# Optimization experiments

Hardware: AMD Instinct MI355X
Metric: run time of the kernel (lower is better)

The kernel has to match this reference:

```python
import jax, jax.numpy as jnp
import numpy as np

DIM = 1024
SEQ = 4096


def setup_inputs() -> dict:
    key = jax.random.key(0)
    ks = jax.random.split(key, 7)
    s = 1.0 / np.sqrt(DIM)
    return {
        "X": jax.random.normal(ks[0], (SEQ, DIM), dtype=jnp.float32),
        "Wq": jax.random.uniform(ks[1], (DIM, DIM), jnp.float32, -s, s),
        "bq": jax.random.uniform(ks[2], (DIM,), jnp.float32, -s, s),
        "Wk": jax.random.uniform(ks[3], (DIM, DIM), jnp.float32, -s, s),
        "bk": jax.random.uniform(ks[4], (DIM,), jnp.float32, -s, s),
        "Wv": jax.random.uniform(ks[5], (DIM, DIM), jnp.float32, -s, s),
        "bv": jax.random.uniform(ks[6], (DIM,), jnp.float32, -s, s),
    }


def reference(X, Wq, bq, Wk, bk, Wv, bv):
    # QKV projections (nn.Linear: x @ W.T + b); here W stored as [in, out]
    Q = X @ Wq + bq            # [S, D]
    K = X @ Wk + bk            # [S, D]
    V = X @ Wv + bv            # [S, D]
    scale = 1.0 / jnp.sqrt(jnp.asarray(X.shape[-1], X.dtype))
    scores = (Q @ K.T) * scale  # [S, S]
    attn = jax.nn.softmax(scores, axis=-1)
    return attn @ V            # [S, D]
```

## Files before the change

### kernel.cpp

```cpp
#include <hip/hip_runtime.h>

typedef unsigned short u16;
typedef unsigned int u32;
typedef __bf16 bf16x8 __attribute__((ext_vector_type(8)));
typedef float f32x4 __attribute__((ext_vector_type(4)));
typedef u16 u16x4 __attribute__((ext_vector_type(4)));

__device__ __forceinline__ u16 f32_to_bf16(float f) {
    u32 u = __builtin_bit_cast(u32, f);
    u32 r = (u + 0x7fffu + ((u >> 16) & 1u)) >> 16;
    return (u16)r;
}

__device__ __forceinline__ float bf16_to_f32(u16 h) {
    u32 u = (u32)h << 16;
    return __builtin_bit_cast(float, u);
}

__device__ __forceinline__ void async_cp16(const u16* g, u16* l) {
    __builtin_amdgcn_global_load_lds(
        (const __attribute__((address_space(1))) u32*)g,
        (__attribute__((address_space(3))) u32*)l, 16, 0, 0);
}

#define G2_DECL(Aptr, Bptr, LDA, LDB, KLEN)                                   \
    __shared__ u16 lds[65536];                                                \
    const int tid  = threadIdx.x;                                             \
    const int wid  = tid >> 6;                                                \
    const int lane = tid & 63;                                                \
    const int wr = wid >> 2;                 \
    const int wc = wid & 3;                  \
    const int row16 = lane & 15;                                              \
    const int quad  = lane >> 4;                                              \
    const int sc0 = (quad * 8) ^ ((row16 & 7) * 8);       \
    const int gr = lane >> 3;                           \
    const int gc = ((lane & 7) ^ gr) * 8;               \
    const int blk0 = wid * 2, blk1 = blk0 + 1;                                \
    const size_t ldaS = (LDA), ldbS = (LDB);                                  \
    const u16* gA = (Aptr) + (size_t)(bm + gr) * ldaS + gc;                   \
    const u16* gB = (Bptr) + (size_t)(bn + gr) * ldbS + gc;                   \
    const int NT = (KLEN) >> 6;                                               \
    f32x4 acc[8][4];                                                          \
    {                                                                         \
        const f32x4 z_ = {0.f, 0.f, 0.f, 0.f};                                \
        _Pragma("unroll")                                                     \
        for (int i_ = 0; i_ < 8; i_++)                                        \
            _Pragma("unroll")                                                 \
            for (int j_ = 0; j_ < 4; j_++) acc[i_][j_] = z_;                  \
    }

#define G2_STAGE(bsel) {                                                      \
    u16* l_ = &lds[(bsel) * 32768];                                           \
    async_cp16(gA + (size_t)(blk0 * 8) * ldaS,       l_ + blk0 * 512);        \
    async_cp16(gA + (size_t)(blk1 * 8) * ldaS,       l_ + blk1 * 512);        \
    async_cp16(gA + (size_t)(128 + blk0 * 8) * ldaS, l_ + 8192 + blk0 * 512); \
    async_cp16(gA + (size_t)(128 + blk1 * 8) * ldaS, l_ + 8192 + blk1 * 512); \
    async_cp16(gB + (size_t)(blk0 * 8) * ldbS,       l_ + 16384 + blk0 * 512);\
    async_cp16(gB + (size_t)(blk1 * 8) * ldbS,       l_ + 16384 + blk1 * 512);\
    async_cp16(gB + (size_t)(128 + blk0 * 8) * ldbS, l_ + 24576 + blk0 * 512);\
    async_cp16(gB + (size_t)(128 + blk1 * 8) * ldbS, l_ + 24576 + blk1 * 512);\
    gA += 64; gB += 64; }

#define G2_LA(cb, im, sc) \
    (*(const bf16x8*)&lds[(cb) + wr * 8192 + (im) * 1024 + row16 * 64 + (sc)])
#define G2_LB(cb, in, sc) \
    (*(const bf16x8*)&lds[(cb) + 16384 + wc * 4096 + (in) * 1024 + row16 * 64 + (sc)])

#define G2_MMA(IM0, JN0, FB)                                                  \
    _Pragma("unroll")                                                         \
    for (int i_m = 0; i_m < 4; i_m++)                                         \
        _Pragma("unroll")                                                     \
        for (int j_n = 0; j_n < 2; j_n++) {                                   \
            acc[(IM0) + i_m][(JN0) + j_n] =                                   \
                __builtin_amdgcn_mfma_f32_16x16x32_bf16(                      \
                    fa[i_m][0], FB[j_n][0], acc[(IM0) + i_m][(JN0) + j_n],    \
                    0, 0, 0);                                                 \
            acc[(IM0) + i_m][(JN0) + j_n] =                                   \
                __builtin_amdgcn_mfma_f32_16x16x32_bf16(                      \
                    fa[i_m][1], FB[j_n][1], acc[(IM0) + i_m][(JN0) + j_n],    \
                    0, 0, 0);                                                 \
        }

#define G2_KLOOP()                                                            \
    G2_STAGE(0)                                                               \
    G2_STAGE(1)                                                               \
    for (int t = 0; t < NT; t++) {                                            \
        const int cb = (t & 1) * 32768;                                       \
        if (t < NT - 1) { asm volatile("s_waitcnt vmcnt(8)" ::: "memory"); }  \
        else            { asm volatile("s_waitcnt vmcnt(0)" ::: "memory"); }  \
        __builtin_amdgcn_s_barrier();                                         \
        bf16x8 fa[4][2], f0[2][2], f1[2][2];                                  \
                                 \
        _Pragma("unroll")                                                     \
        for (int i = 0; i < 4; i++) {                                         \
            fa[i][0] = G2_LA(cb, i, sc0);                                     \
            fa[i][1] = G2_LA(cb, i, sc0 ^ 32);                                \
        }                                                                     \
        _Pragma("unroll")                                                     \
        for (int j = 0; j < 2; j++) {                                         \
            f0[j][0] = G2_LB(cb, j, sc0);                                     \
            f0[j][1] = G2_LB(cb, j, sc0 ^ 32);                                \
        }                                                                     \
        __builtin_amdgcn_s_barrier();                                         \
        __builtin_amdgcn_s_setprio(1);                                        \
        G2_MMA(0, 0, f0)                                                      \
        __builtin_amdgcn_s_setprio(0);                                        \
        __builtin_amdgcn_s_barrier();                                         \
                                           \
        _Pragma("unroll")                                                     \
        for (int j = 0; j < 2; j++) {                                         \
            f1[j][0] = G2_LB(cb, 2 + j, sc0);                                 \
            f1[j][1] = G2_LB(cb, 2 + j, sc0 ^ 32);                            \
        }                                                                     \
        __builtin_amdgcn_s_barrier();                                         \
        __builtin_amdgcn_s_setprio(1);                                        \
        G2_MMA(0, 2, f1)                                                      \
        __builtin_amdgcn_s_setprio(0);                                        \
        __builtin_amdgcn_s_barrier();                                         \
                               \
        _Pragma("unroll")                                                     \
        for (int i = 0; i < 4; i++) {                                         \
            fa[i][0] = G2_LA(cb, 4 + i, sc0);                                 \
            fa[i][1] = G2_LA(cb, 4 + i, sc0 ^ 32);                            \
        }                                                                     \
        __builtin_amdgcn_s_barrier();                                         \
        __builtin_amdgcn_s_setprio(1);                                        \
        G2_MMA(4, 2, f1)                                                      \
        __builtin_amdgcn_s_setprio(0);                                        \
        __builtin_amdgcn_s_barrier();                                         \
                                    \
        _Pragma("unroll")                                                     \
        for (int j = 0; j < 2; j++) {                                         \
            f0[j][0] = G2_LB(cb, j, sc0);                                     \
            f0[j][1] = G2_LB(cb, j, sc0 ^ 32);                                \
        }                                                                     \
        __builtin_amdgcn_s_barrier();                                         \
        __builtin_amdgcn_s_setprio(1);                                        \
        G2_MMA(4, 0, f0)                                                      \
        __builtin_amdgcn_s_setprio(0);                                        \
        asm volatile("s_waitcnt lgkmcnt(0)" ::: "memory");                    \
        __builtin_amdgcn_s_barrier();                                         \
        if (t + 2 < NT) { G2_STAGE((t & 1)) }                                 \
    }

__global__ __launch_bounds__(512, 2)
void gemm_qkv(const u16* __restrict__ A, const u16* __restrict__ B,
              u16* __restrict__ C, u16* __restrict__ Vt,
              const float* __restrict__ bias,
              int K, int lda, int ldb, int ldc)
{
    const int L  = blockIdx.x;
    const int wg = (L & 7) * 24 + (L >> 3);
    const int bm = (wg / 12) * 256;
    const int bn = (wg % 12) * 256;
    G2_DECL(A, B, lda, ldb, K)
    G2_KLOOP()
    if (bn < 2048) {
        #pragma unroll
        for (int im = 0; im < 8; im++) {
            #pragma unroll
            for (int in = 0; in < 4; in++) {
                const int n = bn + wc * 64 + in * 16 + row16;
                const float bv = bias[n];
                #pragma unroll
                for (int r = 0; r < 4; r++) {
                    const int m = bm + wr * 128 + im * 16 + quad * 4 + r;
                    C[(size_t)m * ldc + n] = f32_to_bf16(acc[im][in][r] + bv);
                }
            }
        }
    } else {
        #pragma unroll
        for (int im = 0; im < 8; im++) {
            #pragma unroll
            for (int in = 0; in < 4; in++) {
                const int n = bn + wc * 64 + in * 16 + row16;
                const float bv = bias[n];
                const int d = n - 2048;
                const int m = bm + wr * 128 + im * 16 + quad * 4;
                u16x4 pk;
                #pragma unroll
                for (int r = 0; r < 4; r++)
                    pk[r] = f32_to_bf16(acc[im][in][r] + bv);
                *(u16x4*)&Vt[(size_t)d * 4096 + m] = pk;
            }
        }
    }
}

__global__ __launch_bounds__(512, 2)
void gemm_score_exp(const u16* __restrict__ A, const u16* __restrict__ B,
                    u16* __restrict__ P, float* __restrict__ rowsum,
                    int K, int lda, int ldb, int ldc, float scale)
{
    const int L = blockIdx.x;
    const int xcd = L & 7, q = L >> 3;
    const int bm = ((xcd >> 1) * 4 + (q >> 3)) * 256;
    const int bn = ((xcd & 1) * 8 + (q & 7)) * 256;
    G2_DECL(A, B, lda, ldb, K)
    G2_KLOOP()
    #pragma unroll
    for (int im = 0; im < 8; im++) {
        #pragma unroll
        for (int r = 0; r < 4; r++) {
            const int m = bm + wr * 128 + im * 16 + quad * 4 + r;
            float rs = 0.f;
            #pragma unroll
            for (int in = 0; in < 4; in++) {
                const int n = bn + wc * 64 + in * 16 + row16;
                float e = __expf(acc[im][in][r] * scale);
                P[(size_t)m * ldc + n] = f32_to_bf16(e);
                rs += e;
            }
            rs += __shfl_xor(rs, 1);
            rs += __shfl_xor(rs, 2);
            rs += __shfl_xor(rs, 4);
            rs += __shfl_xor(rs, 8);
            if (row16 == 0) atomicAdd(&rowsum[m], rs);
        }
    }
}

__global__ __launch_bounds__(512, 2)
void gemm_pv_splitk(const u16* __restrict__ A, const u16* __restrict__ B,
                    u16* __restrict__ P0, u16* __restrict__ P1,
                    u16* __restrict__ P2, u16* __restrict__ P3,
                    int Kq, int lda, int ldb, int ldc)
{
    const int L = blockIdx.x;
    const int xcd = L & 7, q = L >> 3;
    const int bm = ((xcd >> 1) * 4 + (q & 3)) * 256;
    const int bn = ((xcd & 1) * 2 + (q >> 2)) * 256;
    const int z  = blockIdx.y;
    u16* C = (z == 0) ? P0 : (z == 1) ? P1 : (z == 2) ? P2 : P3;
    const int koff = z * Kq;
    G2_DECL(A + koff, B + koff, lda, ldb, Kq)
    G2_KLOOP()
    #pragma unroll
    for (int im = 0; im < 8; im++) {
        #pragma unroll
        for (int in = 0; in < 4; in++) {
            const int n = bn + wc * 64 + in * 16 + row16;
            #pragma unroll
            for (int r = 0; r < 4; r++) {
                const int m = bm + wr * 128 + im * 16 + quad * 4 + r;
                C[(size_t)m * ldc + n] = f32_to_bf16(acc[im][in][r]);
            }
        }
    }
}

__global__ __launch_bounds__(256)
void reduce4_scale(float4* __restrict__ out, const u16x4* __restrict__ p0,
                   const u16x4* __restrict__ p1, const u16x4* __restrict__ p2,
                   const u16x4* __restrict__ p3, const float* __restrict__ rowsum)
{
    const int i = blockIdx.x * 256 + threadIdx.x;
    const float inv = 1.0f / rowsum[i >> 8];
    u16x4 a = p0[i], b = p1[i], c = p2[i], d = p3[i];
    float4 o;
    o.x = (bf16_to_f32(a[0]) + bf16_to_f32(b[0]) + bf16_to_f32(c[0]) + bf16_to_f32(d[0])) * inv;
    o.y = (bf16_to_f32(a[1]) + bf16_to_f32(b[1]) + bf16_to_f32(c[1]) + bf16_to_f32(d[1])) * inv;
    o.z = (bf16_to_f32(a[2]) + bf16_to_f32(b[2]) + bf16_to_f32(c[2]) + bf16_to_f32(d[2])) * inv;
    o.w = (bf16_to_f32(a[3]) + bf16_to_f32(b[3]) + bf16_to_f32(c[3]) + bf16_to_f32(d[3])) * inv;
    out[i] = o;
}

__global__ __launch_bounds__(256)
void prep_all(const float4* __restrict__ X, uint2* __restrict__ Xb,
              const float* __restrict__ W0, const float* __restrict__ W1,
              const float* __restrict__ W2, u16* __restrict__ Wt,
              const float* __restrict__ bq, const float* __restrict__ bk,
              const float* __restrict__ bv, float* __restrict__ b3,
              float* __restrict__ rowsum)
{
    __shared__ float t[32][33];
    const int b = blockIdx.x;
    if (b < 4096) {
        const int i = b * 256 + threadIdx.x;
        float4 v = X[i];
        uint2 o;
        o.x = (u32)f32_to_bf16(v.x) | ((u32)f32_to_bf16(v.y) << 16);
        o.y = (u32)f32_to_bf16(v.z) | ((u32)f32_to_bf16(v.w) << 16);
        Xb[i] = o;
    } else if (b < 7168) {
        const int tt = b - 4096;
        const int z  = tt >> 10;
        const int r  = tt & 1023;
        const float* W = (z == 0) ? W0 : (z == 1) ? W1 : W2;
        u16* dst = Wt + (size_t)z * 1024 * 1024;
        const int bk2 = (r & 31) * 32;
        const int bn2 = (r >> 5) * 32;
        const int tx = threadIdx.x & 31;
        const int ty = threadIdx.x >> 5;
        #pragma unroll
        for (int i = 0; i < 32; i += 8)
            t[ty + i][tx] = W[(size_t)(bk2 + ty + i) * 1024 + bn2 + tx];
        __syncthreads();
        #pragma unroll
        for (int i = 0; i < 32; i += 8)
            dst[(size_t)(bn2 + ty + i) * 1024 + bk2 + tx] = f32_to_bf16(t[tx][ty + i]);
    } else {
        const int i = (b - 7168) * 256 + threadIdx.x;
        if (i < 3072)
            b3[i] = (i < 1024) ? bq[i] : (i < 2048) ? bk[i - 1024] : bv[i - 2048];
        else
            rowsum[i - 3072] = 0.f;
    }
}

extern "C" void kernel_launch(void* const* d_in, const int* in_sizes, int n_in,
                              void* d_out, int out_size, void* d_ws, size_t ws_size,
                              hipStream_t stream)
{
    const float* X  = (const float*)d_in[0];
    const float* Wq = (const float*)d_in[1];
    const float* bq = (const float*)d_in[2];
    const float* Wk = (const float*)d_in[3];
    const float* bk = (const float*)d_in[4];
    const float* Wv = (const float*)d_in[5];
    const float* bv = (const float*)d_in[6];
    float* out = (float*)d_out;

    char* ws = (char*)d_ws;
    u16*   P      = (u16*)ws;
    u16*   Xb     = (u16*)ws;
    u16*   WqkvT  = (u16*)(ws + (8u << 20));
    float* rowsum = (float*)(ws + (32u << 20));
    float* bias3  = (float*)(ws + (32u << 20) + (64u << 10));
    u16*   QKV    = (u16*)(ws + (33u << 20));
    u16*   p0     = (u16*)(ws + (33u << 20));
    u16*   p1     = (u16*)(ws + (41u << 20));
    u16*   p2     = (u16*)(ws + (49u << 20));
    u16*   p3     = (u16*)(ws + (57u << 20));
    u16*   Vt     = (u16*)(ws + (65u << 20));

    prep_all<<<7196, 256, 0, stream>>>((const float4*)X, (uint2*)Xb,
        Wq, Wk, Wv, WqkvT, bq, bk, bv, bias3, rowsum);

    gemm_qkv<<<192, 512, 0, stream>>>(Xb, WqkvT, QKV, Vt, bias3,
        1024, 1024, 1024, 3072);

    gemm_score_exp<<<256, 512, 0, stream>>>(QKV, QKV + 1024, P, rowsum,
        1024, 3072, 3072, 4096, 0.03125f);

    gemm_pv_splitk<<<dim3(64, 4), 512, 0, stream>>>(P, Vt, p0, p1, p2, p3,
        1024, 4096, 4096, 1024);

    reduce4_scale<<<4096, 256, 0, stream>>>((float4*)out, (const u16x4*)p0,
        (const u16x4*)p1, (const u16x4*)p2, (const u16x4*)p3, rowsum);
}
```

Measured before the change: 222.3 us.

## Interleave next-tile async loads across MMA phases and reuse B fragments

Restructures the GEMM K-loop so that the global-to-LDS copies for the next tile are spread across the three MFMA phases of the current tile, instead of being issued in a batch at the end of each iteration with two tiles in flight. The loop is unrolled by two with fixed LDS buffer offsets. The fourth phase now reuses the f0 fragments already held in registers instead of reloading them from LDS, which removes one LDS read pass and one barrier. The trade-off is that prefetch depth drops from two tiles to one, and each tile ends with a full vmcnt(0) wait, which can expose global load latency.

```diff
diff --git a/kernel.cpp b/kernel.cpp
--- a/kernel.cpp
+++ b/kernel.cpp
@@ -49,17 +49,10 @@
             for (int j_ = 0; j_ < 4; j_++) acc[i_][j_] = z_;                  \
     }
 
-#define G2_STAGE(bsel) {                                                      \
-    u16* l_ = &lds[(bsel) * 32768];                                           \
-    async_cp16(gA + (size_t)(blk0 * 8) * ldaS,       l_ + blk0 * 512);        \
-    async_cp16(gA + (size_t)(blk1 * 8) * ldaS,       l_ + blk1 * 512);        \
-    async_cp16(gA + (size_t)(128 + blk0 * 8) * ldaS, l_ + 8192 + blk0 * 512); \
-    async_cp16(gA + (size_t)(128 + blk1 * 8) * ldaS, l_ + 8192 + blk1 * 512); \
-    async_cp16(gB + (size_t)(blk0 * 8) * ldbS,       l_ + 16384 + blk0 * 512);\
-    async_cp16(gB + (size_t)(blk1 * 8) * ldbS,       l_ + 16384 + blk1 * 512);\
-    async_cp16(gB + (size_t)(128 + blk0 * 8) * ldbS, l_ + 24576 + blk0 * 512);\
-    async_cp16(gB + (size_t)(128 + blk1 * 8) * ldbS, l_ + 24576 + blk1 * 512);\
-    gA += 64; gB += 64; }
+#define G2_ST_A(NB, R, LOFF) \
+    async_cp16(gA + (size_t)(R) * ldaS, &lds[(NB) + (LOFF)]);
+#define G2_ST_B(NB, R, LOFF) \
+    async_cp16(gB + (size_t)(R) * ldbS, &lds[(NB) + 16384 + (LOFF)]);
 
 #define G2_LA(cb, im, sc) \
     (*(const bf16x8*)&lds[(cb) + wr * 8192 + (im) * 1024 + row16 * 64 + (sc)])
@@ -81,66 +74,86 @@
                     0, 0, 0);                                                 \
         }
 
-#define G2_KLOOP()                                                            \
-    G2_STAGE(0)                                                               \
-    G2_STAGE(1)                                                               \
-    for (int t = 0; t < NT; t++) {                                            \
-        const int cb = (t & 1) * 32768;                                       \
-        if (t < NT - 1) { asm volatile("s_waitcnt vmcnt(8)" ::: "memory"); }  \
-        else            { asm volatile("s_waitcnt vmcnt(0)" ::: "memory"); }  \
-        __builtin_amdgcn_s_barrier();                                         \
+#define G2_TILE(CB, NB, SCOND)                                                \
+    {                                                                         \
         bf16x8 fa[4][2], f0[2][2], f1[2][2];                                  \
-                                 \
+          \
         _Pragma("unroll")                                                     \
         for (int i = 0; i < 4; i++) {                                         \
-            fa[i][0] = G2_LA(cb, i, sc0);                                     \
-            fa[i][1] = G2_LA(cb, i, sc0 ^ 32);                                \
+            fa[i][0] = G2_LA(CB, i, sc0);                                     \
+            fa[i][1] = G2_LA(CB, i, sc0 ^ 32);                                \
         }                                                                     \
         _Pragma("unroll")                                                     \
         for (int j = 0; j < 2; j++) {                                         \
-            f0[j][0] = G2_LB(cb, j, sc0);                                     \
-            f0[j][1] = G2_LB(cb, j, sc0 ^ 32);                                \
+            f0[j][0] = G2_LB(CB, j, sc0);                                     \
+            f0[j][1] = G2_LB(CB, j, sc0 ^ 32);                                \
+        }                                                                     \
+        if (SCOND) {                                                          \
+            G2_ST_A(NB, blk0 * 8, blk0 * 512)                                 \
+            G2_ST_A(NB, blk1 * 8, blk1 * 512)                                 \
+            G2_ST_A(NB, 128 + blk0 * 8, 8192 + blk0 * 512)                    \
         }                                                                     \
         __builtin_amdgcn_s_barrier();                                         \
         __builtin_amdgcn_s_setprio(1);                                        \
         G2_MMA(0, 0, f0)                                                      \
         __builtin_amdgcn_s_setprio(0);                                        \
         __builtin_amdgcn_s_barrier();                                         \
-                                           \
+                  \
         _Pragma("unroll")                                                     \
         for (int j = 0; j < 2; j++) {                                         \
-            f1[j][0] = G2_LB(cb, 2 + j, sc0);                                 \
-            f1[j][1] = G2_LB(cb, 2 + j, sc0 ^ 32);                            \
+            f1[j][0] = G2_LB(CB, 2 + j, sc0);                                 \
+            f1[j][1] = G2_LB(CB, 2 + j, sc0 ^ 32);                            \
+        }                                                                     \
+        if (SCOND) {                                                          \
+            G2_ST_A(NB, 128 + blk1 * 8, 8192 + blk1 * 512)                    \
+            G2_ST_B(NB, blk0 * 8, blk0 * 512)                                 \
+            G2_ST_B(NB, blk1 * 8, blk1 * 512)                                 \
         }                                                                     \
         __builtin_amdgcn_s_barrier();                                         \
         __builtin_amdgcn_s_setprio(1);                                        \
         G2_MMA(0, 2, f1)                                                      \
         __builtin_amdgcn_s_setprio(0);                                        \
         __builtin_amdgcn_s_barrier();                                         \
-                               \
+                  \
         _Pragma("unroll")                                                     \
         for (int i = 0; i < 4; i++) {                                         \
-            fa[i][0] = G2_LA(cb, 4 + i, sc0);                                 \
-            fa[i][1] = G2_LA(cb, 4 + i, sc0 ^ 32);                            \
+            fa[i][0] = G2_LA(CB, 4 + i, sc0);                                 \
+            fa[i][1] = G2_LA(CB, 4 + i, sc0 ^ 32);                            \
+        }                                                                     \
+        if (SCOND) {                                                          \
+            G2_ST_B(NB, 128 + blk0 * 8, 8192 + blk0 * 512)                    \
+            G2_ST_B(NB, 128 + blk1 * 8, 8192 + blk1 * 512)                    \
+            gA += 64; gB += 64;                                               \
         }                                                                     \
         __builtin_amdgcn_s_barrier();                                         \
         __builtin_amdgcn_s_setprio(1);                                        \
         G2_MMA(4, 2, f1)                                                      \
         __builtin_amdgcn_s_setprio(0);                                        \
         __builtin_amdgcn_s_barrier();                                         \
-                                    \
-        _Pragma("unroll")                                                     \
-        for (int j = 0; j < 2; j++) {                                         \
-            f0[j][0] = G2_LB(cb, j, sc0);                                     \
-            f0[j][1] = G2_LB(cb, j, sc0 ^ 32);                                \
-        }                                                                     \
-        __builtin_amdgcn_s_barrier();                                         \
+             \
         __builtin_amdgcn_s_setprio(1);                                        \
         G2_MMA(4, 0, f0)                                                      \
         __builtin_amdgcn_s_setprio(0);                                        \
-        asm volatile("s_waitcnt lgkmcnt(0)" ::: "memory");                    \
-        __builtin_amdgcn_s_barrier();                                         \
-        if (t + 2 < NT) { G2_STAGE((t & 1)) }                                 \
+        asm volatile("s_waitcnt vmcnt(0)" ::: "memory");                      \
+        __builtin_amdgcn_s_barrier();                                         \
+    }
+
+#define G2_KLOOP()                                                            \
+                           \
+    G2_ST_A(0, blk0 * 8, blk0 * 512)                                          \
+    G2_ST_A(0, blk1 * 8, blk1 * 512)                                          \
+    G2_ST_A(0, 128 + blk0 * 8, 8192 + blk0 * 512)                             \
+    G2_ST_A(0, 128 + blk1 * 8, 8192 + blk1 * 512)                             \
+    G2_ST_B(0, blk0 * 8, blk0 * 512)                                          \
+    G2_ST_B(0, blk1 * 8, blk1 * 512)                                          \
+    G2_ST_B(0, 128 + blk0 * 8, 8192 + blk0 * 512)                             \
+    G2_ST_B(0, 128 + blk1 * 8, 8192 + blk1 * 512)                             \
+    gA += 64; gB += 64;                                                       \
+    asm volatile("s_waitcnt vmcnt(0)" ::: "memory");                          \
+    __builtin_amdgcn_s_barrier();                                             \
+    for (int t2 = 0; t2 < NT; t2 += 2) {                                      \
+        G2_TILE(0, 32768, (t2 + 1 < NT))                                      \
+        G2_TILE(32768, 0, (t2 + 2 < NT))                                      \
     }
 
 __global__ __launch_bounds__(512, 2)
```

Measured after the change: 203.6 us. 1.09x faster.
